# Performance work log

Hardware: AMD Instinct MI355X
Metric: run time of the kernel (lower is better)

Reference implementation:

```python
import jax, jax.numpy as jnp
import numpy as np

N = 50000   # nodes
E = 600000  # edges
D = 128     # in_channels
H = 32      # MLP hidden


def setup_inputs() -> dict:
    key = jax.random.key(0)
    ks = jax.random.split(key, 10)
    x = jax.random.normal(ks[0], (N, D), dtype=jnp.float32)
    edge_index = jax.random.randint(ks[1], (2, E), 0, N, dtype=jnp.int32)
    W_gcn = jax.random.normal(ks[2], (D, D), dtype=jnp.float32) / np.sqrt(D)
    b_gcn = jnp.zeros((D,), dtype=jnp.float32)
    w1 = jax.random.normal(ks[3], (D, H), dtype=jnp.float32) / np.sqrt(D)
    b1 = jnp.zeros((H,), dtype=jnp.float32)
    w2 = jax.random.normal(ks[4], (H, H), dtype=jnp.float32) / np.sqrt(H)
    b2 = jnp.zeros((H,), dtype=jnp.float32)
    w3 = jax.random.normal(ks[5], (H, 1), dtype=jnp.float32) / np.sqrt(H)
    b3 = jnp.zeros((1,), dtype=jnp.float32)
    return {"x": x, "edge_index": edge_index, "W_gcn": W_gcn, "b_gcn": b_gcn,
            "w1": w1, "b1": b1, "w2": w2, "b2": b2, "w3": w3, "b3": b3}


def _gcn_conv(x, edge_index, W, b):
    """PyG GCNConv: add self-loops, symmetric D^-1/2 (A+I) D^-1/2 normalization."""
    xw = x @ W  # [N, D]
    loop = jnp.arange(N, dtype=edge_index.dtype)
    row = jnp.concatenate([edge_index[0], loop])  # source
    col = jnp.concatenate([edge_index[1], loop])  # target
    deg = jax.ops.segment_sum(jnp.ones_like(col, dtype=xw.dtype), col, num_segments=N)
    dinv = jnp.where(deg > 0, jax.lax.rsqrt(deg), 0.0)
    norm = dinv[row] * dinv[col]              # [E+N]
    msg = xw[row] * norm[:, None]             # gather + scale, [E+N, D]
    out = jax.ops.segment_sum(msg, col, num_segments=N)  # scatter-add, [N, D]
    return out + b


def reference(x, edge_index, W_gcn, b_gcn, w1, b1, w2, b2, w3, b3):
    out = jax.nn.relu(_gcn_conv(x, edge_index, W_gcn, b_gcn))
    h = out + x                               # residual
    h = jax.nn.relu(h @ w1 + b1)
    h = jax.nn.relu(h @ w2 + b2)
    return h @ w3 + b3                        # [N, 1]
```

## Files before the change

### kernel.cpp

```cpp
#include <hip/hip_runtime.h>

#define DIM 128
#define HID 32
#define CAP 64

typedef __attribute__((ext_vector_type(8))) short v8s;
typedef __attribute__((ext_vector_type(8))) unsigned short v8u;
typedef __attribute__((ext_vector_type(4))) float v4f;
typedef __attribute__((ext_vector_type(4))) int v4i;

static __device__ __forceinline__ unsigned short f2bf(float f) {
    unsigned int u = __float_as_uint(f);
    u += 0x7fffu + ((u >> 16) & 1u);
    return (unsigned short)(u >> 16);
}

__global__ __launch_bounds__(256) void prep_kernel(int* __restrict__ cnt,
                                                   const float* __restrict__ W,
                                                   unsigned short* __restrict__ wbt,
                                                   int n, int nz) {
    int t = threadIdx.x;
    if ((int)blockIdx.x < nz) {
        int i0 = (blockIdx.x << 10) + t * 4;
        if (i0 + 3 < n) {
            *(int4*)&cnt[i0] = make_int4(0, 0, 0, 0);
        } else {
            for (int i = i0; i < n; ++i) cnt[i] = 0;
        }
    } else {
        int base = (blockIdx.x - nz) * 2048 + t * 8;
#pragma unroll
        for (int i = 0; i < 8; ++i) {
            int f = base + i;
            int k = f >> 7, nn = f & 127;
            wbt[nn * 128 + k] = f2bf(W[f]);
        }
    }
}

__global__ __launch_bounds__(256) void fill_kernel(const int* __restrict__ ei,
                                                   int* __restrict__ cnt,
                                                   int* __restrict__ srcs, int E) {
    int t = threadIdx.x;
    const int* col = ei + E;
    int base = ((int)blockIdx.x * 256 + t) * 8;
    if (base + 7 < E) {
        v4i ra = __builtin_nontemporal_load((const v4i*)&ei[base]);
        v4i rb = __builtin_nontemporal_load((const v4i*)&ei[base + 4]);
        v4i ca = __builtin_nontemporal_load((const v4i*)&col[base]);
        v4i cb = __builtin_nontemporal_load((const v4i*)&col[base + 4]);
        int p0 = atomicAdd(&cnt[ca[0]], 1);
        int p1 = atomicAdd(&cnt[ca[1]], 1);
        int p2 = atomicAdd(&cnt[ca[2]], 1);
        int p3 = atomicAdd(&cnt[ca[3]], 1);
        int p4 = atomicAdd(&cnt[cb[0]], 1);
        int p5 = atomicAdd(&cnt[cb[1]], 1);
        int p6 = atomicAdd(&cnt[cb[2]], 1);
        int p7 = atomicAdd(&cnt[cb[3]], 1);
        if (p0 < CAP) __builtin_nontemporal_store(ra[0], &srcs[(ca[0] << 6) + p0]);
        if (p1 < CAP) __builtin_nontemporal_store(ra[1], &srcs[(ca[1] << 6) + p1]);
        if (p2 < CAP) __builtin_nontemporal_store(ra[2], &srcs[(ca[2] << 6) + p2]);
        if (p3 < CAP) __builtin_nontemporal_store(ra[3], &srcs[(ca[3] << 6) + p3]);
        if (p4 < CAP) __builtin_nontemporal_store(rb[0], &srcs[(cb[0] << 6) + p4]);
        if (p5 < CAP) __builtin_nontemporal_store(rb[1], &srcs[(cb[1] << 6) + p5]);
        if (p6 < CAP) __builtin_nontemporal_store(rb[2], &srcs[(cb[2] << 6) + p6]);
        if (p7 < CAP) __builtin_nontemporal_store(rb[3], &srcs[(cb[3] << 6) + p7]);
    } else {
        for (int e = base; e < E; ++e) {
            int r = ei[e], c = col[e];
            int p = atomicAdd(&cnt[c], 1);
            if (p < CAP) srcs[(c << 6) + p] = r;
        }
    }
}

__global__ __launch_bounds__(256) void gemm_kernel(const float* __restrict__ x,
                                                   const unsigned short* __restrict__ wbt,
                                                   signed char* __restrict__ xwq,
                                                   float* __restrict__ sc,
                                                   int n) {
    int t = threadIdx.x;
    int row0 = (int)blockIdx.x * 64;
    int w = t >> 6;
    int l = t & 63;
    int q = l >> 4;
    int mn = l & 15;
    int row = row0 + w * 16 + mn;

    v8s afrag[4];
    const float* xr = x + (size_t)row * DIM + q * 8;
#pragma unroll
    for (int kt = 0; kt < 4; ++kt) {
        float4 qa = make_float4(0.f, 0.f, 0.f, 0.f), qb = qa;
        if (row < n) {
            const float4* s4 = (const float4*)(xr + kt * 32);
            qa = s4[0];
            qb = s4[1];
        }
        v8u pk;
        pk[0] = f2bf(qa.x); pk[1] = f2bf(qa.y); pk[2] = f2bf(qa.z); pk[3] = f2bf(qa.w);
        pk[4] = f2bf(qb.x); pk[5] = f2bf(qb.y); pk[6] = f2bf(qb.z); pk[7] = f2bf(qb.w);
        afrag[kt] = (v8s)pk;
    }

    v4f acc[8];
    const unsigned short* wr = wbt + mn * 128 + q * 8;
#pragma unroll
    for (int ct = 0; ct < 8; ++ct) {
        acc[ct] = (v4f){0.f, 0.f, 0.f, 0.f};
#pragma unroll
        for (int kt = 0; kt < 4; ++kt) {
            v8s bfrag = *(const v8s*)(wr + ct * (16 * 128) + kt * 32);
            acc[ct] = __builtin_amdgcn_mfma_f32_16x16x32_bf16(afrag[kt], bfrag, acc[ct], 0, 0, 0);
        }
    }

    float m[4];
#pragma unroll
    for (int i = 0; i < 4; ++i) {
        float mm = 0.f;
#pragma unroll
        for (int ct = 0; ct < 8; ++ct) mm = fmaxf(mm, fabsf(acc[ct][i]));
        m[i] = mm;
    }
#pragma unroll
    for (int off = 1; off < 16; off <<= 1) {
#pragma unroll
        for (int i = 0; i < 4; ++i) m[i] = fmaxf(m[i], __shfl_xor(m[i], off));
    }
    float inv[4];
#pragma unroll
    for (int i = 0; i < 4; ++i) {
        m[i] = fmaxf(m[i], 1e-20f);
        inv[i] = 127.0f / m[i];
    }
    if (mn == 0) {
#pragma unroll
        for (int i = 0; i < 4; ++i) {
            int rowg = row0 + w * 16 + q * 4 + i;
            if (rowg < n) sc[rowg] = m[i] * (1.0f / 127.0f);
        }
    }
#pragma unroll
    for (int ct = 0; ct < 8; ++ct) {
        int colg = ct * 16 + mn;
#pragma unroll
        for (int i = 0; i < 4; ++i) {
            int rowg = row0 + w * 16 + q * 4 + i;
            if (rowg < n)
                xwq[(size_t)rowg * DIM + colg] =
                    (signed char)__float2int_rn(acc[ct][i] * inv[i]);
        }
    }
}

__global__ __launch_bounds__(256) void dw_kernel(const int* __restrict__ cnt,
                                                 const float* __restrict__ sc,
                                                 float* __restrict__ dw, int n) {
    int i0 = (blockIdx.x * 256 + threadIdx.x) * 4;
    if (i0 + 3 < n) {
        int4 c4 = *(const int4*)&cnt[i0];
        float4 s4 = *(const float4*)&sc[i0];
        float4 w4;
        w4.x = rsqrtf((float)c4.x + 1.0f) * s4.x;
        w4.y = rsqrtf((float)c4.y + 1.0f) * s4.y;
        w4.z = rsqrtf((float)c4.z + 1.0f) * s4.z;
        w4.w = rsqrtf((float)c4.w + 1.0f) * s4.w;
        *(float4*)&dw[i0] = w4;
    } else {
        for (int i = i0; i < n; ++i) dw[i] = rsqrtf((float)cnt[i] + 1.0f) * sc[i];
    }
}

__global__ __launch_bounds__(256) void gather_tail_kernel(
    const signed char* __restrict__ xwq, const float* __restrict__ x,
    const int* __restrict__ cnt, const int* __restrict__ srcs,
    const float* __restrict__ dw, const float* __restrict__ sc,
    const float* __restrict__ b_gcn,
    const float* __restrict__ w1, const float* __restrict__ b1,
    const float* __restrict__ w2, const float* __restrict__ b2,
    const float* __restrict__ w3, const float* __restrict__ b3,
    float* __restrict__ out, int n) {
    __shared__ float hs[8][132];
    __shared__ float t1s[8][40];
    int t = threadIdx.x;
    int g = t >> 5, j = t & 31;
    int node = blockIdx.x * 8 + g;

    if (node < n) {
        int d = min(cnt[node], CAP);
        int beg = node << 6;
        int aq = ((const int*)(xwq + (size_t)node * DIM))[j];
        float scn = sc[node];
        float4 xv = ((const float4*)(x + (size_t)node * DIM))[j];
        float4 bg = ((const float4*)b_gcn)[j];
        float ax = 0.f, ay = 0.f, az = 0.f, aw = 0.f;
        for (int c0 = 0; c0 < d; c0 += 32) {
            int sj = 0; float wj = 0.f;
            if (c0 + j < d) {
                sj = srcs[beg + c0 + j];
                wj = dw[sj];
            }
            int m = min(32, d - c0);
            for (int i = 0; i < m; i += 8) {
                int v[8]; float wgt[8];
#pragma unroll
                for (int u = 0; u < 8; ++u) {
                    int src = __shfl(sj, i + u, 32);
                    wgt[u] = __shfl(wj, i + u, 32);
                    v[u] = ((const int*)(xwq + (size_t)src * DIM))[j];
                }
#pragma unroll
                for (int u = 0; u < 8; ++u) {
                    ax += wgt[u] * (float)((v[u] << 24) >> 24);
                    ay += wgt[u] * (float)((v[u] << 16) >> 24);
                    az += wgt[u] * (float)((v[u] <<  8) >> 24);
                    aw += wgt[u] * (float)( v[u]        >> 24);
                }
            }
        }
        float di = rsqrtf((float)d + 1.0f);
        float sself = di * di * scn;
        float* h = &hs[g][4 * j];
        h[0] = fmaxf(di * ax + sself * (float)((aq << 24) >> 24) + bg.x, 0.f) + xv.x;
        h[1] = fmaxf(di * ay + sself * (float)((aq << 16) >> 24) + bg.y, 0.f) + xv.y;
        h[2] = fmaxf(di * az + sself * (float)((aq <<  8) >> 24) + bg.z, 0.f) + xv.z;
        h[3] = fmaxf(di * aw + sself * (float)( aq        >> 24) + bg.w, 0.f) + xv.w;
        float acc = b1[j];
        for (int k = 0; k < DIM; k += 4) {
            float4 hv = *(const float4*)&hs[g][k];
            acc += hv.x * w1[(k + 0) * HID + j];
            acc += hv.y * w1[(k + 1) * HID + j];
            acc += hv.z * w1[(k + 2) * HID + j];
            acc += hv.w * w1[(k + 3) * HID + j];
        }
        t1s[g][j] = fmaxf(acc, 0.0f);
        acc = b2[j];
        for (int k = 0; k < HID; k += 4) {
            float4 tv = *(const float4*)&t1s[g][k];
            acc += tv.x * w2[(k + 0) * HID + j];
            acc += tv.y * w2[(k + 1) * HID + j];
            acc += tv.z * w2[(k + 2) * HID + j];
            acc += tv.w * w2[(k + 3) * HID + j];
        }
        float v = fmaxf(acc, 0.0f) * w3[j];
#pragma unroll
        for (int off = 16; off > 0; off >>= 1) v += __shfl_down(v, off, 32);
        if (j == 0) out[node] = v + b3[0];
    }
}

extern "C" void kernel_launch(void* const* d_in, const int* in_sizes, int n_in,
                              void* d_out, int out_size, void* d_ws, size_t ws_size,
                              hipStream_t stream) {
    const float* x     = (const float*)d_in[0];
    const int*   ei    = (const int*)d_in[1];
    const float* W_gcn = (const float*)d_in[2];
    const float* b_gcn = (const float*)d_in[3];
    const float* w1    = (const float*)d_in[4];
    const float* b1    = (const float*)d_in[5];
    const float* w2    = (const float*)d_in[6];
    const float* b2    = (const float*)d_in[7];
    const float* w3    = (const float*)d_in[8];
    const float* b3    = (const float*)d_in[9];
    float* out = (float*)d_out;

    const int n = in_sizes[0] / DIM;
    const int E = in_sizes[1] / 2;

    char* ws = (char*)d_ws;
    signed char* xwq = (signed char*)ws;
    char* p = ws + (size_t)n * DIM;
    p = (char*)(((size_t)p + 15) & ~(size_t)15);
    float* sc   = (float*)p;         p += (size_t)n * sizeof(float);
    float* dw   = (float*)p;         p += (size_t)n * sizeof(float);
    int*   cnt  = (int*)p;           p += (size_t)n * sizeof(int);
    p = (char*)(((size_t)p + 255) & ~(size_t)255);
    int*   srcs = (int*)p;           p += (size_t)n * CAP * sizeof(int);
    unsigned short* wbt = (unsigned short*)p;

    const int nz     = (n + 1023) / 1024;
    const int ngemm  = (n + 63) / 64;
    const int nfill  = (E + 2047) / 2048;

    prep_kernel<<<nz + 8, 256, 0, stream>>>(cnt, W_gcn, wbt, n, nz);
    fill_kernel<<<nfill, 256, 0, stream>>>(ei, cnt, srcs, E);
    gemm_kernel<<<ngemm, 256, 0, stream>>>(x, wbt, xwq, sc, n);
    dw_kernel<<<(n + 1023) / 1024, 256, 0, stream>>>(cnt, sc, dw, n);
    gather_tail_kernel<<<(n + 7) / 8, 256, 0, stream>>>(xwq, x, cnt, srcs, dw, sc,
                                                        b_gcn, w1, b1, w2, b2,
                                                        w3, b3, out, n);
}
```

Baseline: 189.1 us.

## Fuse edge fill into GEMM launch with XCD-partitioned atomics, drop dw kernel

The CSR-fill and GEMM kernels become one launch: the first 512 blocks bucket edges, and the rest run the MFMA GEMM tiles. Each fill block only handles destination nodes whose low 3 bits match its block index mod 8, aiming to keep atomics on a node's counter within one XCD's L2. The per-node dw kernel is removed and its weight is computed on the fly in the gather. In exchange, each fill block reads every edge in its slice, so edge-index reads grow eightfold, and the gather does an extra cnt load per neighbor.

Measured after the change: 171.1 us. 1.11x faster.

```diff
diff --git a/kernel.cpp b/kernel.cpp
--- a/kernel.cpp
+++ b/kernel.cpp
@@ -3,6 +3,7 @@
 #define DIM 128
 #define HID 32
 #define CAP 64
+#define NFILL 512
 
 typedef __attribute__((ext_vector_type(8))) short v8s;
 typedef __attribute__((ext_vector_type(8))) unsigned short v8u;
@@ -18,165 +19,145 @@
 __global__ __launch_bounds__(256) void prep_kernel(int* __restrict__ cnt,
                                                    const float* __restrict__ W,
                                                    unsigned short* __restrict__ wbt,
-                                                   int n, int nz) {
+                                                   int n) {
+    int gtid = (int)blockIdx.x * 256 + threadIdx.x;
+    int nthr = (int)gridDim.x * 256;
+    for (int i = gtid * 4; i < n; i += nthr * 4) {
+        if (i + 3 < n) {
+            *(int4*)&cnt[i] = make_int4(0, 0, 0, 0);
+        } else {
+            for (int k = i; k < n; ++k) cnt[k] = 0;
+        }
+    }
+    for (int f = gtid; f < DIM * DIM; f += nthr) {
+        int k = f >> 7, nn = f & 127;
+        wbt[nn * 128 + k] = f2bf(W[f]);
+    }
+}
+
+__global__ __launch_bounds__(256, 4) void gemm_fill_kernel(const float* __restrict__ x,
+                                                           const unsigned short* __restrict__ wbt,
+                                                           signed char* __restrict__ xwq,
+                                                           float* __restrict__ sc,
+                                                           const int* __restrict__ ei,
+                                                           int* __restrict__ cnt,
+                                                           int* __restrict__ srcs,
+                                                           int n, int E) {
     int t = threadIdx.x;
-    if ((int)blockIdx.x < nz) {
-        int i0 = (blockIdx.x << 10) + t * 4;
-        if (i0 + 3 < n) {
-            *(int4*)&cnt[i0] = make_int4(0, 0, 0, 0);
-        } else {
-            for (int i = i0; i < n; ++i) cnt[i] = 0;
+    int b = (int)blockIdx.x;
+    if (b < NFILL) {
+        const int* col = ei + E;
+        const int xcd = b & 7;
+        const int s = b >> 3;
+        const int nslice = NFILL >> 3;
+        const int quads = (E + 3) >> 2;
+        const int qps = (quads + nslice - 1) / nslice;
+        const int q0 = s * qps;
+        const int q1 = min(q0 + qps, quads);
+        for (int qi = q0 + t; qi < q1; qi += 256) {
+            int base = qi * 4;
+            if (base + 3 < E) {
+                v4i r = __builtin_nontemporal_load((const v4i*)&ei[base]);
+                v4i c = __builtin_nontemporal_load((const v4i*)&col[base]);
+#pragma unroll
+                for (int u = 0; u < 4; ++u) {
+                    int cc = c[u];
+                    if ((cc & 7) == xcd) {
+                        int p = atomicAdd(&cnt[cc], 1);
+                        if (p < CAP) srcs[(cc << 6) + p] = r[u];
+                    }
+                }
+            } else {
+                for (int e = base; e < E; ++e) {
+                    int cc = col[e];
+                    if ((cc & 7) == xcd) {
+                        int p = atomicAdd(&cnt[cc], 1);
+                        if (p < CAP) srcs[(cc << 6) + p] = ei[e];
+                    }
+                }
+            }
         }
     } else {
-        int base = (blockIdx.x - nz) * 2048 + t * 8;
-#pragma unroll
-        for (int i = 0; i < 8; ++i) {
-            int f = base + i;
-            int k = f >> 7, nn = f & 127;
-            wbt[nn * 128 + k] = f2bf(W[f]);
-        }
-    }
-}
-
-__global__ __launch_bounds__(256) void fill_kernel(const int* __restrict__ ei,
-                                                   int* __restrict__ cnt,
-                                                   int* __restrict__ srcs, int E) {
-    int t = threadIdx.x;
-    const int* col = ei + E;
-    int base = ((int)blockIdx.x * 256 + t) * 8;
-    if (base + 7 < E) {
-        v4i ra = __builtin_nontemporal_load((const v4i*)&ei[base]);
-        v4i rb = __builtin_nontemporal_load((const v4i*)&ei[base + 4]);
-        v4i ca = __builtin_nontemporal_load((const v4i*)&col[base]);
-        v4i cb = __builtin_nontemporal_load((const v4i*)&col[base + 4]);
-        int p0 = atomicAdd(&cnt[ca[0]], 1);
-        int p1 = atomicAdd(&cnt[ca[1]], 1);
-        int p2 = atomicAdd(&cnt[ca[2]], 1);
-        int p3 = atomicAdd(&cnt[ca[3]], 1);
-        int p4 = atomicAdd(&cnt[cb[0]], 1);
-        int p5 = atomicAdd(&cnt[cb[1]], 1);
-        int p6 = atomicAdd(&cnt[cb[2]], 1);
-        int p7 = atomicAdd(&cnt[cb[3]], 1);
-        if (p0 < CAP) __builtin_nontemporal_store(ra[0], &srcs[(ca[0] << 6) + p0]);
-        if (p1 < CAP) __builtin_nontemporal_store(ra[1], &srcs[(ca[1] << 6) + p1]);
-        if (p2 < CAP) __builtin_nontemporal_store(ra[2], &srcs[(ca[2] << 6) + p2]);
-        if (p3 < CAP) __builtin_nontemporal_store(ra[3], &srcs[(ca[3] << 6) + p3]);
-        if (p4 < CAP) __builtin_nontemporal_store(rb[0], &srcs[(cb[0] << 6) + p4]);
-        if (p5 < CAP) __builtin_nontemporal_store(rb[1], &srcs[(cb[1] << 6) + p5]);
-        if (p6 < CAP) __builtin_nontemporal_store(rb[2], &srcs[(cb[2] << 6) + p6]);
-        if (p7 < CAP) __builtin_nontemporal_store(rb[3], &srcs[(cb[3] << 6) + p7]);
-    } else {
-        for (int e = base; e < E; ++e) {
-            int r = ei[e], c = col[e];
-            int p = atomicAdd(&cnt[c], 1);
-            if (p < CAP) srcs[(c << 6) + p] = r;
-        }
-    }
-}
-
-__global__ __launch_bounds__(256) void gemm_kernel(const float* __restrict__ x,
-                                                   const unsigned short* __restrict__ wbt,
-                                                   signed char* __restrict__ xwq,
-                                                   float* __restrict__ sc,
-                                                   int n) {
-    int t = threadIdx.x;
-    int row0 = (int)blockIdx.x * 64;
-    int w = t >> 6;
-    int l = t & 63;
-    int q = l >> 4;
-    int mn = l & 15;
-    int row = row0 + w * 16 + mn;
-
-    v8s afrag[4];
-    const float* xr = x + (size_t)row * DIM + q * 8;
-#pragma unroll
-    for (int kt = 0; kt < 4; ++kt) {
-        float4 qa = make_float4(0.f, 0.f, 0.f, 0.f), qb = qa;
-        if (row < n) {
-            const float4* s4 = (const float4*)(xr + kt * 32);
-            qa = s4[0];
-            qb = s4[1];
-        }
-        v8u pk;
-        pk[0] = f2bf(qa.x); pk[1] = f2bf(qa.y); pk[2] = f2bf(qa.z); pk[3] = f2bf(qa.w);
-        pk[4] = f2bf(qb.x); pk[5] = f2bf(qb.y); pk[6] = f2bf(qb.z); pk[7] = f2bf(qb.w);
-        afrag[kt] = (v8s)pk;
-    }
-
-    v4f acc[8];
-    const unsigned short* wr = wbt + mn * 128 + q * 8;
-#pragma unroll
-    for (int ct = 0; ct < 8; ++ct) {
-        acc[ct] = (v4f){0.f, 0.f, 0.f, 0.f};
+        int tile = b - NFILL;
+        int row0 = tile * 64;
+        int w = t >> 6;
+        int l = t & 63;
+        int q = l >> 4;
+        int mn = l & 15;
+        int row = row0 + w * 16 + mn;
+
+        v8s afrag[4];
+        const float* xr = x + (size_t)row * DIM + q * 8;
 #pragma unroll
         for (int kt = 0; kt < 4; ++kt) {
-            v8s bfrag = *(const v8s*)(wr + ct * (16 * 128) + kt * 32);
-            acc[ct] = __builtin_amdgcn_mfma_f32_16x16x32_bf16(afrag[kt], bfrag, acc[ct], 0, 0, 0);
-        }
-    }
-
-    float m[4];
-#pragma unroll
-    for (int i = 0; i < 4; ++i) {
-        float mm = 0.f;
-#pragma unroll
-        for (int ct = 0; ct < 8; ++ct) mm = fmaxf(mm, fabsf(acc[ct][i]));
-        m[i] = mm;
-    }
-#pragma unroll
-    for (int off = 1; off < 16; off <<= 1) {
-#pragma unroll
-        for (int i = 0; i < 4; ++i) m[i] = fmaxf(m[i], __shfl_xor(m[i], off));
-    }
-    float inv[4];
-#pragma unroll
-    for (int i = 0; i < 4; ++i) {
-        m[i] = fmaxf(m[i], 1e-20f);
-        inv[i] = 127.0f / m[i];
-    }
-    if (mn == 0) {
+            float4 qa = make_float4(0.f, 0.f, 0.f, 0.f), qb = qa;
+            if (row < n) {
+                const float4* s4 = (const float4*)(xr + kt * 32);
+                qa = s4[0];
+                qb = s4[1];
+            }
+            v8u pk;
+            pk[0] = f2bf(qa.x); pk[1] = f2bf(qa.y); pk[2] = f2bf(qa.z); pk[3] = f2bf(qa.w);
+            pk[4] = f2bf(qb.x); pk[5] = f2bf(qb.y); pk[6] = f2bf(qb.z); pk[7] = f2bf(qb.w);
+            afrag[kt] = (v8s)pk;
+        }
+
+        v4f acc[8];
+        const unsigned short* wr = wbt + mn * 128 + q * 8;
+#pragma unroll
+        for (int ct = 0; ct < 8; ++ct) {
+            acc[ct] = (v4f){0.f, 0.f, 0.f, 0.f};
+#pragma unroll
+            for (int kt = 0; kt < 4; ++kt) {
+                v8s bfrag = *(const v8s*)(wr + ct * (16 * 128) + kt * 32);
+                acc[ct] = __builtin_amdgcn_mfma_f32_16x16x32_bf16(afrag[kt], bfrag, acc[ct], 0, 0, 0);
+            }
+        }
+
+        float m[4];
 #pragma unroll
         for (int i = 0; i < 4; ++i) {
-            int rowg = row0 + w * 16 + q * 4 + i;
-            if (rowg < n) sc[rowg] = m[i] * (1.0f / 127.0f);
-        }
-    }
-#pragma unroll
-    for (int ct = 0; ct < 8; ++ct) {
-        int colg = ct * 16 + mn;
+            float mm = 0.f;
+#pragma unroll
+            for (int ct = 0; ct < 8; ++ct) mm = fmaxf(mm, fabsf(acc[ct][i]));
+            m[i] = mm;
+        }
+#pragma unroll
+        for (int off = 1; off < 16; off <<= 1) {
+#pragma unroll
+            for (int i = 0; i < 4; ++i) m[i] = fmaxf(m[i], __shfl_xor(m[i], off));
+        }
+        float inv[4];
 #pragma unroll
         for (int i = 0; i < 4; ++i) {
-            int rowg = row0 + w * 16 + q * 4 + i;
-            if (rowg < n)
-                xwq[(size_t)rowg * DIM + colg] =
-                    (signed char)__float2int_rn(acc[ct][i] * inv[i]);
-        }
-    }
-}
-
-__global__ __launch_bounds__(256) void dw_kernel(const int* __restrict__ cnt,
-                                                 const float* __restrict__ sc,
-                                                 float* __restrict__ dw, int n) {
-    int i0 = (blockIdx.x * 256 + threadIdx.x) * 4;
-    if (i0 + 3 < n) {
-        int4 c4 = *(const int4*)&cnt[i0];
-        float4 s4 = *(const float4*)&sc[i0];
-        float4 w4;
-        w4.x = rsqrtf((float)c4.x + 1.0f) * s4.x;
-        w4.y = rsqrtf((float)c4.y + 1.0f) * s4.y;
-        w4.z = rsqrtf((float)c4.z + 1.0f) * s4.z;
-        w4.w = rsqrtf((float)c4.w + 1.0f) * s4.w;
-        *(float4*)&dw[i0] = w4;
-    } else {
-        for (int i = i0; i < n; ++i) dw[i] = rsqrtf((float)cnt[i] + 1.0f) * sc[i];
+            m[i] = fmaxf(m[i], 1e-20f);
+            inv[i] = 127.0f / m[i];
+        }
+        if (mn == 0) {
+#pragma unroll
+            for (int i = 0; i < 4; ++i) {
+                int rowg = row0 + w * 16 + q * 4 + i;
+                if (rowg < n) sc[rowg] = m[i] * (1.0f / 127.0f);
+            }
+        }
+#pragma unroll
+        for (int ct = 0; ct < 8; ++ct) {
+            int colg = ct * 16 + mn;
+#pragma unroll
+            for (int i = 0; i < 4; ++i) {
+                int rowg = row0 + w * 16 + q * 4 + i;
+                if (rowg < n)
+                    xwq[(size_t)rowg * DIM + colg] =
+                        (signed char)__float2int_rn(acc[ct][i] * inv[i]);
+            }
+        }
     }
 }
 
 __global__ __launch_bounds__(256) void gather_tail_kernel(
     const signed char* __restrict__ xwq, const float* __restrict__ x,
     const int* __restrict__ cnt, const int* __restrict__ srcs,
-    const float* __restrict__ dw, const float* __restrict__ sc,
-    const float* __restrict__ b_gcn,
+    const float* __restrict__ sc, const float* __restrict__ b_gcn,
     const float* __restrict__ w1, const float* __restrict__ b1,
     const float* __restrict__ w2, const float* __restrict__ b2,
     const float* __restrict__ w3, const float* __restrict__ b3,
@@ -199,7 +180,7 @@
             int sj = 0; float wj = 0.f;
             if (c0 + j < d) {
                 sj = srcs[beg + c0 + j];
-                wj = dw[sj];
+                wj = rsqrtf((float)cnt[sj] + 1.0f) * sc[sj];
             }
             int m = min(32, d - c0);
             for (int i = 0; i < m; i += 8) {
@@ -273,21 +254,17 @@
     char* p = ws + (size_t)n * DIM;
     p = (char*)(((size_t)p + 15) & ~(size_t)15);
     float* sc   = (float*)p;         p += (size_t)n * sizeof(float);
-    float* dw   = (float*)p;         p += (size_t)n * sizeof(float);
     int*   cnt  = (int*)p;           p += (size_t)n * sizeof(int);
     p = (char*)(((size_t)p + 255) & ~(size_t)255);
     int*   srcs = (int*)p;           p += (size_t)n * CAP * sizeof(int);
     unsigned short* wbt = (unsigned short*)p;
 
-    const int nz     = (n + 1023) / 1024;
-    const int ngemm  = (n + 63) / 64;
-    const int nfill  = (E + 2047) / 2048;
-
-    prep_kernel<<<nz + 8, 256, 0, stream>>>(cnt, W_gcn, wbt, n, nz);
-    fill_kernel<<<nfill, 256, 0, stream>>>(ei, cnt, srcs, E);
-    gemm_kernel<<<ngemm, 256, 0, stream>>>(x, wbt, xwq, sc, n);
-    dw_kernel<<<(n + 1023) / 1024, 256, 0, stream>>>(cnt, sc, dw, n);
-    gather_tail_kernel<<<(n + 7) / 8, 256, 0, stream>>>(xwq, x, cnt, srcs, dw, sc,
+    const int ngemm = (n + 63) / 64;
+
+    prep_kernel<<<64, 256, 0, stream>>>(cnt, W_gcn, wbt, n);
+    gemm_fill_kernel<<<NFILL + ngemm, 256, 0, stream>>>(x, wbt, xwq, sc, ei,
+                                                        cnt, srcs, n, E);
+    gather_tail_kernel<<<(n + 7) / 8, 256, 0, stream>>>(xwq, x, cnt, srcs, sc,
                                                         b_gcn, w1, b1, w2, b2,
                                                         w3, b3, out, n);
 }
```
